# Kernel tuning notes

Measured on AMD Instinct MI355X. Metric: run time of the kernel, lower is better.

The kernel has to match this reference:

```python
import jax, jax.numpy as jnp
import numpy as np

B, T, D = 64, 2048, 256


def setup_inputs() -> dict:
    key = jax.random.key(0)
    k0, k1, k2, k3 = jax.random.split(key, 4)
    x0 = jax.random.normal(k0, (B, D), dtype=jnp.float32)
    I = jax.random.normal(k1, (B, T, D), dtype=jnp.float32)
    # Scale transition matrix so spectral norm < 1 (stable 2048-step recurrence),
    # mimicking eW = expm((W - I)*dt/tau) which is contractive for stable W.
    eW = jax.random.normal(k2, (D, D), dtype=jnp.float32) * (0.9 / np.sqrt(D))
    W_inv_eW = jax.random.normal(k3, (D, D), dtype=jnp.float32) * (1.0 / np.sqrt(D))
    return {"x0": x0, "I": I, "eW": eW, "W_inv_eW": W_inv_eW}


def reference(x0, I, eW, W_inv_eW):
    # x[:,0]=x0; x[:,t] = x[:,t-1] @ eW.T + I[:,t-1] @ W_inv_eW.T
    u = jnp.einsum('btd,sd->bts', I, W_inv_eW)  # [B, T, D], precompute input drive

    def step(x, u_t):
        x_new = x @ eW.T + u_t  # [B, D]
        return x_new, x_new

    # only u[:, :T-1] is consumed (x[:,t] uses I[:,t-1])
    _, xs = jax.lax.scan(step, x0, jnp.swapaxes(u[:, :-1], 0, 1))  # xs: [T-1, B, D]
    x = jnp.concatenate([x0[:, None, :], jnp.swapaxes(xs, 0, 1)], axis=1)  # [B, T, D]
    return x
```

## Files before the change

### kernel.cpp

```cpp
#include <hip/hip_runtime.h>
#include <stdint.h>
#include <stddef.h>


#define BATCH 64
#define TLEN 2048
#define DDIM 256
#define CHUNK 32
#define NCHUNK 64

typedef __attribute__((ext_vector_type(8))) short short8;
typedef __attribute__((ext_vector_type(4))) short short4_t;
typedef __attribute__((ext_vector_type(4))) float f32x4;

#define MFMA16(a, b, c) __builtin_amdgcn_mfma_f32_16x16x32_bf16((a), (b), (c), 0, 0, 0)
#define PIN8(x) asm volatile("" : "+v"(x))

__device__ __forceinline__ uint16_t f2bf(float f) {
  union { float f; uint32_t u; } v; v.f = f;
  return (uint16_t)((v.u + 0x7fffu + ((v.u >> 16) & 1u)) >> 16);
}
__device__ __forceinline__ float bf2f(uint16_t h) {
  union { uint32_t u; float f; } v; v.u = ((uint32_t)h) << 16;
  return v.f;
}

__device__ __forceinline__ void split8(const float* fv, short8& hi, short8& lo) {
#pragma unroll
  for (int j = 0; j < 8; ++j) {
    uint16_t hb = f2bf(fv[j]);
    hi[j] = (short)hb;
    lo[j] = (short)f2bf(fv[j] - bf2f(hb));
  }
}

__device__ __forceinline__ uint32_t swz(int row) {
  return ((uint32_t)((row & 7) << 4)) ^ ((uint32_t)(((row >> 3) & 1) << 7));
}

__device__ __forceinline__ void wg_barrier() {
  __builtin_amdgcn_sched_barrier(0);
  asm volatile("s_waitcnt lgkmcnt(0)" ::: "memory");
  __builtin_amdgcn_s_barrier();
  asm volatile("" ::: "memory");
  __builtin_amdgcn_sched_barrier(0);
}

#define WS_A_HI   (0)
#define WS_A_LO   (128 * 1024)
#define WS_WB_HI  (256 * 1024)
#define WS_WB_LO  (384 * 1024)
#define WS_M1F    (512 * 1024)
#define WS_M1_HI  (768 * 1024)
#define WS_M1_LO  (896 * 1024)
#define WS_M2F    (1024 * 1024)
#define WS_M2_HI  (1280 * 1024)
#define WS_M2_LO  (1408 * 1024)
#define WS_M3F    (1536 * 1024)
#define WS_M3_HI  (1792 * 1024)
#define WS_M3_LO  (1920 * 1024)
#define WS_ATF    (2048 * 1024)
#define WS_CNT    (2304 * 1024)
#define WS_S      (2560 * 1024)
#define WS_Y      (6656 * 1024)

__global__ void k_split(const float* __restrict__ eW, const float* __restrict__ Wi,
                        uint16_t* __restrict__ Ah, uint16_t* __restrict__ Al,
                        uint16_t* __restrict__ Wh, uint16_t* __restrict__ Wl,
                        float* __restrict__ AtF, unsigned int* __restrict__ cnt) {
  int idx = blockIdx.x * blockDim.x + threadIdx.x;
  if (idx == 0) *cnt = 0u;
  if (idx < 65536) {
    float v = eW[idx];
    uint16_t h = f2bf(v);
    Ah[idx] = h;
    Al[idx] = f2bf(v - bf2f(h));
    AtF[(idx & 255) * 256 + (idx >> 8)] = v;
  } else if (idx < 131072) {
    int i = idx - 65536;
    float v = Wi[i];
    uint16_t h = f2bf(v);
    Wh[i] = h;
    Wl[i] = f2bf(v - bf2f(h));
  }
}

__global__ __launch_bounds__(512) void k_power(
    const float* __restrict__ AtF, const uint16_t* __restrict__ Ah, const uint16_t* __restrict__ Al,
    float* __restrict__ M1f, uint16_t* __restrict__ M1h, uint16_t* __restrict__ M1l,
    float* __restrict__ M2f, uint16_t* __restrict__ M2h, uint16_t* __restrict__ M2l,
    float* __restrict__ M3f, uint16_t* __restrict__ M3h, uint16_t* __restrict__ M3l,
    unsigned int* __restrict__ cnt) {
  const int mf = blockIdx.x;
  const int tid = threadIdx.x;
  const int w = tid >> 6, l = tid & 63, l15 = l & 15, quad = l >> 4;
  const int ns = w * 32;

  auto mm = [&](const float* Af, const uint16_t* Bh, const uint16_t* Bl,
                float* Of, uint16_t* Oh, uint16_t* Ol) {
    f32x4 acc[2];
    acc[0] = {0.f, 0.f, 0.f, 0.f};
    acc[1] = {0.f, 0.f, 0.f, 0.f};
#pragma unroll
    for (int ks = 0; ks < 8; ++ks) {
      const float* ap = Af + (size_t)(mf * 16 + l15) * 256 + ks * 32 + quad * 8;
      f32x4 f0 = *reinterpret_cast<const f32x4*>(ap);
      f32x4 f1 = *reinterpret_cast<const f32x4*>(ap + 4);
      float fv[8] = {f0[0], f0[1], f0[2], f0[3], f1[0], f1[1], f1[2], f1[3]};
      short8 ah, al8;
      split8(fv, ah, al8);
#pragma unroll
      for (int nf = 0; nf < 2; ++nf) {
        const int off = (ns + nf * 16 + l15) * 256 + ks * 32 + quad * 8;
        short8 bhf = *reinterpret_cast<const short8*>(Bh + off);
        short8 blf = *reinterpret_cast<const short8*>(Bl + off);
        acc[nf] = MFMA16(ah, bhf, acc[nf]);
        acc[nf] = MFMA16(al8, bhf, acc[nf]);
        acc[nf] = MFMA16(ah, blf, acc[nf]);
      }
    }
#pragma unroll
    for (int nf = 0; nf < 2; ++nf)
#pragma unroll
      for (int r = 0; r < 4; ++r) {
        int row = mf * 16 + quad * 4 + r;
        int col = ns + nf * 16 + l15;
        float v = acc[nf][r];
        Of[(size_t)row * 256 + col] = v;
        uint16_t hb = f2bf(v);
        Oh[(size_t)col * 256 + row] = hb;
        Ol[(size_t)col * 256 + row] = f2bf(v - bf2f(hb));
      }
  };

  unsigned int target = 0;
  auto gbar = [&]() {
    __syncthreads();
    target += 16;
    if (tid == 0) {
      __hip_atomic_fetch_add(cnt, 1u, __ATOMIC_RELEASE, __HIP_MEMORY_SCOPE_AGENT);
      while (__hip_atomic_load(cnt, __ATOMIC_ACQUIRE, __HIP_MEMORY_SCOPE_AGENT) < target) {
      }
    }
    __syncthreads();
  };

  mm(AtF, Ah, Al, M2f, M2h, M2l);    gbar();
  mm(M2f, M2h, M2l, M3f, M3h, M3l);  gbar();
  mm(M3f, M3h, M3l, M2f, M2h, M2l);  gbar();
  mm(M2f, M2h, M2l, M3f, M3h, M3l);  gbar();
  mm(M3f, M3h, M3l, M1f, M1h, M1l);  gbar();
  mm(M1f, M1h, M1l, M2f, M2h, M2l);  gbar();
  mm(M2f, M1h, M1l, M3f, M3h, M3l);
}

__global__ __launch_bounds__(1024, 1) void k_u(const float* __restrict__ I,
                                               const uint16_t* __restrict__ Wh,
                                               const uint16_t* __restrict__ Wl,
                                               float* __restrict__ out) {
  const int tid = threadIdx.x;
  const int w = tid >> 6, l = tid & 63, l15 = l & 15, quad = l >> 4;
  const int ns = w * 16;
  __shared__ __align__(16) uint16_t sIh[2][4096];
  __shared__ __align__(16) uint16_t sIl[2][4096];

  short8 bh[8], bl[8];
#pragma unroll
  for (int ks = 0; ks < 8; ++ks) {
    const int off = (ns + l15) * 256 + ks * 32 + quad * 8;
    bh[ks] = *reinterpret_cast<const short8*>(Wh + off);
    bl[ks] = *reinterpret_cast<const short8*>(Wl + off);
    PIN8(bh[ks]);
    PIN8(bl[ks]);
  }

  const int srow = tid >> 6;
  const int sc0 = (tid & 63) * 4;
  const uint32_t wbyte = ((uint32_t)(srow * 512 + sc0 * 2)) ^ swz(srow);

  f32x4 ra, rb, rc, rd;
  auto loadI = [&](int tl, f32x4& dst) {
    const int b = tl >> 7, tt = tl & 127;
    dst = *reinterpret_cast<const f32x4*>(I + ((size_t)b * TLEN + tt * 16 + srow) * DDIM + sc0);
  };

  auto do_tile = [&](int tl, f32x4& cur, f32x4& pf, int q, bool pre) {
    if (pre) loadI(tl + 512, pf);
    short4_t hi4, lo4;
#pragma unroll
    for (int j = 0; j < 4; ++j) {
      uint16_t hb = f2bf(cur[j]);
      hi4[j] = (short)hb;
      lo4[j] = (short)f2bf(cur[j] - bf2f(hb));
    }
    *reinterpret_cast<short4_t*>(reinterpret_cast<char*>(sIh[q]) + wbyte) = hi4;
    *reinterpret_cast<short4_t*>(reinterpret_cast<char*>(sIl[q]) + wbyte) = lo4;
    wg_barrier();
    const int b = tl >> 7, tt = tl & 127;
    f32x4 acc = {0.f, 0.f, 0.f, 0.f};
    __builtin_amdgcn_s_setprio(1);
#pragma unroll
    for (int ks = 0; ks < 8; ++ks) {
      uint32_t rbyte = ((uint32_t)(l15 * 512 + ks * 64 + quad * 16)) ^ swz(l15);
      short8 ih = *reinterpret_cast<const short8*>((const char*)sIh[q] + rbyte);
      short8 il = *reinterpret_cast<const short8*>((const char*)sIl[q] + rbyte);
      acc = MFMA16(ih, bh[ks], acc);
      acc = MFMA16(il, bh[ks], acc);
      acc = MFMA16(ih, bl[ks], acc);
    }
    __builtin_amdgcn_s_setprio(0);
#pragma unroll
    for (int r = 0; r < 4; ++r) {
      int trow = tt * 16 + quad * 4 + r;
      if (trow <= TLEN - 2) {
        out[((size_t)b * TLEN + trow + 1) * DDIM + ns + l15] = acc[r];
      }
    }
  };

  const int tl0 = blockIdx.x;
  loadI(tl0, ra);
  loadI(tl0 + 256, rb);
#pragma unroll 1
  for (int it = 0; it < 32; it += 4) {
    do_tile(tl0 + (it + 0) * 256, ra, rc, 0, it + 2 < 32);
    do_tile(tl0 + (it + 1) * 256, rb, rd, 1, it + 3 < 32);
    do_tile(tl0 + (it + 2) * 256, rc, ra, 0, it + 4 < 32);
    do_tile(tl0 + (it + 3) * 256, rd, rb, 1, it + 5 < 32);
  }
}

__global__ __launch_bounds__(1024) void k_scan(const int pass,
                                               const uint16_t* __restrict__ Ah,
                                               const uint16_t* __restrict__ Al,
                                               float* __restrict__ xu,
                                               const float* __restrict__ Y,
                                               float* __restrict__ S) {
  const int tid = threadIdx.x;
  const int w = tid >> 6, l = tid & 63, l15 = l & 15, quad = l >> 4;
  const int ns = w * 16;
  const int c = blockIdx.x >> 2;
  const int rg = blockIdx.x & 3;
  __shared__ __align__(16) uint16_t sh[2][4096];
  __shared__ __align__(16) uint16_t sl[2][4096];

  const int t0 = c * CHUNK;
  const int nsteps = (t0 + CHUNK <= TLEN - 1) ? CHUNK : (TLEN - 1 - t0);

  float u0[4], u1[4], u2[4], u3[4], fin[4];
#pragma unroll
  for (int j = 0; j < 4; ++j) { u0[j] = 0.f; u1[j] = 0.f; u2[j] = 0.f; u3[j] = 0.f; fin[j] = 0.f; }

  auto issue_u = [&](int i, float (&dst)[4]) {
    if (i > nsteps) return;
#pragma unroll
    for (int r = 0; r < 4; ++r) {
      int b = rg * 16 + quad * 4 + r;
      dst[r] = xu[((size_t)b * TLEN + t0 + i) * DDIM + ns + l15];
    }
  };
  issue_u(1, u0);
  issue_u(2, u1);
  issue_u(3, u2);
  issue_u(4, u3);

  short8 fAh[8], fAl[8];
#pragma unroll
  for (int ks = 0; ks < 8; ++ks) {
    const int off = (ns + l15) * 256 + ks * 32 + quad * 8;
    fAh[ks] = *reinterpret_cast<const short8*>(Ah + off);
    fAl[ks] = *reinterpret_cast<const short8*>(Al + off);
    PIN8(fAh[ks]);
    PIN8(fAl[ks]);
  }

  for (int i = tid; i < 4096; i += 1024) {
    int row = i >> 8, k = i & 255;
    float v;
    if (pass == 1)
      v = 0.0f;
    else {
      v = Y[((size_t)c * 64 + rg * 16 + row) * DDIM + k];
      if (c == 0) xu[((size_t)(rg * 16 + row) * TLEN) * DDIM + k] = v;
    }
    uint16_t hb = f2bf(v);
    uint16_t lb = f2bf(v - bf2f(hb));
    uint32_t byte = ((uint32_t)(row * 512 + k * 2)) ^ swz(row);
    *(uint16_t*)((char*)sh[0] + byte) = hb;
    *(uint16_t*)((char*)sl[0] + byte) = lb;
  }
  wg_barrier();

  int p = 0;
  auto step = [&](int i, float (&ucur)[4]) {
    f32x4 acc = {0.f, 0.f, 0.f, 0.f};
    __builtin_amdgcn_s_setprio(1);
#pragma unroll
    for (int ks = 0; ks < 8; ++ks) {
      uint32_t byte = ((uint32_t)(l15 * 512 + ks * 64 + quad * 16)) ^ swz(l15);
      short8 xh = *reinterpret_cast<const short8*>((const char*)sh[p] + byte);
      short8 xl = *reinterpret_cast<const short8*>((const char*)sl[p] + byte);
      acc = MFMA16(xh, fAh[ks], acc);
      acc = MFMA16(xl, fAh[ks], acc);
      acc = MFMA16(xh, fAl[ks], acc);
    }
    __builtin_amdgcn_s_setprio(0);
#pragma unroll
    for (int r = 0; r < 4; ++r) fin[r] = acc[r] + ucur[r];
    issue_u(i + 4, ucur);
    if (pass == 2) {
#pragma unroll
      for (int r = 0; r < 4; ++r) {
        int b = rg * 16 + quad * 4 + r;
        xu[((size_t)b * TLEN + t0 + i) * DDIM + ns + l15] = fin[r];
      }
    }
    if (i < nsteps) {
#pragma unroll
      for (int r = 0; r < 4; ++r) {
        int row = quad * 4 + r, col = ns + l15;
        float v = fin[r];
        uint16_t hb = f2bf(v);
        uint16_t lb = f2bf(v - bf2f(hb));
        uint32_t byte = ((uint32_t)(row * 512 + col * 2)) ^ swz(row);
        *(uint16_t*)((char*)sh[p ^ 1] + byte) = hb;
        *(uint16_t*)((char*)sl[p ^ 1] + byte) = lb;
      }
      wg_barrier();
      p ^= 1;
    }
  };

  int i = 1;
  for (; i + 3 <= nsteps; i += 4) {
    step(i, u0);
    step(i + 1, u1);
    step(i + 2, u2);
    step(i + 3, u3);
  }
  if (i <= nsteps) { step(i, u0); ++i; }
  if (i <= nsteps) { step(i, u1); ++i; }
  if (i <= nsteps) { step(i, u2); ++i; }

  if (pass == 1) {
#pragma unroll
    for (int r = 0; r < 4; ++r) {
      int row = quad * 4 + r, col = ns + l15;
      S[((size_t)c * 64 + rg * 16 + row) * DDIM + col] = fin[r];
    }
  }
}

__global__ __launch_bounds__(512) void k_bnd(const float* __restrict__ x0,
                                             const float* __restrict__ S,
                                             const uint16_t* __restrict__ M1h, const uint16_t* __restrict__ M1l,
                                             const uint16_t* __restrict__ M2h, const uint16_t* __restrict__ M2l,
                                             const uint16_t* __restrict__ M3h, const uint16_t* __restrict__ M3l,
                                             float* __restrict__ Y) {
  const int c = blockIdx.x;
  const int tid = threadIdx.x;
  const int w = tid >> 6, l = tid & 63, l15 = l & 15, quad = l >> 4;
  const int ns = w * 32;
  f32x4 acc[4][2];
  const float* Tc = (c == 0) ? x0 : (S + (size_t)(c - 1) * 64 * 256);
#pragma unroll
  for (int mf = 0; mf < 4; ++mf)
#pragma unroll
    for (int nf = 0; nf < 2; ++nf)
#pragma unroll
      for (int r = 0; r < 4; ++r)
        acc[mf][nf][r] = Tc[(size_t)(mf * 16 + quad * 4 + r) * 256 + ns + nf * 16 + l15];

  for (int j = 1; j <= 3; ++j) {
    int k = c - j;
    if (k < 0) break;
    const float* Tp = (k == 0) ? x0 : (S + (size_t)(k - 1) * 64 * 256);
    const uint16_t* Bh = (j == 1) ? M1h : (j == 2) ? M2h : M3h;
    const uint16_t* Bl = (j == 1) ? M1l : (j == 2) ? M2l : M3l;
#pragma unroll
    for (int mf = 0; mf < 4; ++mf) {
#pragma unroll
      for (int ks = 0; ks < 8; ++ks) {
        const float* ap = Tp + (size_t)(mf * 16 + l15) * 256 + ks * 32 + quad * 8;
        f32x4 f0 = *reinterpret_cast<const f32x4*>(ap);
        f32x4 f1 = *reinterpret_cast<const f32x4*>(ap + 4);
        float fv[8] = {f0[0], f0[1], f0[2], f0[3], f1[0], f1[1], f1[2], f1[3]};
        short8 ah, al8;
        split8(fv, ah, al8);
#pragma unroll
        for (int nf = 0; nf < 2; ++nf) {
          const int off = (ns + nf * 16 + l15) * 256 + ks * 32 + quad * 8;
          short8 bhf = *reinterpret_cast<const short8*>(Bh + off);
          short8 blf = *reinterpret_cast<const short8*>(Bl + off);
          acc[mf][nf] = MFMA16(ah, bhf, acc[mf][nf]);
          acc[mf][nf] = MFMA16(al8, bhf, acc[mf][nf]);
          acc[mf][nf] = MFMA16(ah, blf, acc[mf][nf]);
        }
      }
    }
  }
#pragma unroll
  for (int mf = 0; mf < 4; ++mf)
#pragma unroll
    for (int nf = 0; nf < 2; ++nf)
#pragma unroll
      for (int r = 0; r < 4; ++r)
        Y[(size_t)c * 64 * 256 + (size_t)(mf * 16 + quad * 4 + r) * 256 + ns + nf * 16 + l15] =
            acc[mf][nf][r];
}

extern "C" void kernel_launch(void* const* d_in, const int* in_sizes, int n_in,
                              void* d_out, int out_size, void* d_ws, size_t ws_size,
                              hipStream_t stream) {
  (void)in_sizes; (void)n_in; (void)out_size; (void)ws_size;
  const float* x0 = (const float*)d_in[0];
  const float* I  = (const float*)d_in[1];
  const float* eW = (const float*)d_in[2];
  const float* Wi = (const float*)d_in[3];
  float* out = (float*)d_out;
  char* ws = (char*)d_ws;

  uint16_t* Ah  = (uint16_t*)(ws + WS_A_HI);
  uint16_t* Al  = (uint16_t*)(ws + WS_A_LO);
  uint16_t* Wh  = (uint16_t*)(ws + WS_WB_HI);
  uint16_t* Wl  = (uint16_t*)(ws + WS_WB_LO);
  float*    M1f = (float*)(ws + WS_M1F);
  uint16_t* M1h = (uint16_t*)(ws + WS_M1_HI);
  uint16_t* M1l = (uint16_t*)(ws + WS_M1_LO);
  float*    M2f = (float*)(ws + WS_M2F);
  uint16_t* M2h = (uint16_t*)(ws + WS_M2_HI);
  uint16_t* M2l = (uint16_t*)(ws + WS_M2_LO);
  float*    M3f = (float*)(ws + WS_M3F);
  uint16_t* M3h = (uint16_t*)(ws + WS_M3_HI);
  uint16_t* M3l = (uint16_t*)(ws + WS_M3_LO);
  float*    AtF = (float*)(ws + WS_ATF);
  unsigned int* cnt = (unsigned int*)(ws + WS_CNT);
  float*    S   = (float*)(ws + WS_S);
  float*    Y   = (float*)(ws + WS_Y);

  k_split<<<512, 256, 0, stream>>>(eW, Wi, Ah, Al, Wh, Wl, AtF, cnt);
  k_power<<<16, 512, 0, stream>>>(AtF, Ah, Al, M1f, M1h, M1l, M2f, M2h, M2l,
                                  M3f, M3h, M3l, cnt);
  k_u<<<256, 1024, 0, stream>>>(I, Wh, Wl, out);
  k_scan<<<256, 1024, 0, stream>>>(1, Ah, Al, out, Y, S);
  k_bnd<<<64, 512, 0, stream>>>(x0, S, M1h, M1l, M2h, M2l, M3h, M3l, Y);
  k_scan<<<256, 1024, 0, stream>>>(2, Ah, Al, out, Y, S);
}
```

Before: 342.3 us.

## Replace persistent power kernel with separate matmul launches and split MFMA accumulators

Removes the persistent k_power kernel, which used an atomic-counter grid barrier, and replaces it with seven k_mm256 launches, with kernel boundaries serving as the global sync. The power chain now launches after k_u rather than before. In k_u and k_scan, the three bf16 split-precision MFMA chains now use separate accumulators that are summed at the end. The separate accumulators break the serial MFMA dependency chain, which shortens latency per scan step. The cost is more kernel launches and slightly different rounding order.

```diff
diff --git a/kernel.cpp b/kernel.cpp
--- a/kernel.cpp
+++ b/kernel.cpp
@@ -60,16 +60,14 @@
 #define WS_M3_HI  (1792 * 1024)
 #define WS_M3_LO  (1920 * 1024)
 #define WS_ATF    (2048 * 1024)
-#define WS_CNT    (2304 * 1024)
 #define WS_S      (2560 * 1024)
 #define WS_Y      (6656 * 1024)
 
 __global__ void k_split(const float* __restrict__ eW, const float* __restrict__ Wi,
                         uint16_t* __restrict__ Ah, uint16_t* __restrict__ Al,
                         uint16_t* __restrict__ Wh, uint16_t* __restrict__ Wl,
-                        float* __restrict__ AtF, unsigned int* __restrict__ cnt) {
+                        float* __restrict__ AtF) {
   int idx = blockIdx.x * blockDim.x + threadIdx.x;
-  if (idx == 0) *cnt = 0u;
   if (idx < 65536) {
     float v = eW[idx];
     uint16_t h = f2bf(v);
@@ -85,75 +83,6 @@
   }
 }
 
-__global__ __launch_bounds__(512) void k_power(
-    const float* __restrict__ AtF, const uint16_t* __restrict__ Ah, const uint16_t* __restrict__ Al,
-    float* __restrict__ M1f, uint16_t* __restrict__ M1h, uint16_t* __restrict__ M1l,
-    float* __restrict__ M2f, uint16_t* __restrict__ M2h, uint16_t* __restrict__ M2l,
-    float* __restrict__ M3f, uint16_t* __restrict__ M3h, uint16_t* __restrict__ M3l,
-    unsigned int* __restrict__ cnt) {
-  const int mf = blockIdx.x;
-  const int tid = threadIdx.x;
-  const int w = tid >> 6, l = tid & 63, l15 = l & 15, quad = l >> 4;
-  const int ns = w * 32;
-
-  auto mm = [&](const float* Af, const uint16_t* Bh, const uint16_t* Bl,
-                float* Of, uint16_t* Oh, uint16_t* Ol) {
-    f32x4 acc[2];
-    acc[0] = {0.f, 0.f, 0.f, 0.f};
-    acc[1] = {0.f, 0.f, 0.f, 0.f};
-#pragma unroll
-    for (int ks = 0; ks < 8; ++ks) {
-      const float* ap = Af + (size_t)(mf * 16 + l15) * 256 + ks * 32 + quad * 8;
-      f32x4 f0 = *reinterpret_cast<const f32x4*>(ap);
-      f32x4 f1 = *reinterpret_cast<const f32x4*>(ap + 4);
-      float fv[8] = {f0[0], f0[1], f0[2], f0[3], f1[0], f1[1], f1[2], f1[3]};
-      short8 ah, al8;
-      split8(fv, ah, al8);
-#pragma unroll
-      for (int nf = 0; nf < 2; ++nf) {
-        const int off = (ns + nf * 16 + l15) * 256 + ks * 32 + quad * 8;
-        short8 bhf = *reinterpret_cast<const short8*>(Bh + off);
-        short8 blf = *reinterpret_cast<const short8*>(Bl + off);
-        acc[nf] = MFMA16(ah, bhf, acc[nf]);
-        acc[nf] = MFMA16(al8, bhf, acc[nf]);
-        acc[nf] = MFMA16(ah, blf, acc[nf]);
-      }
-    }
-#pragma unroll
-    for (int nf = 0; nf < 2; ++nf)
-#pragma unroll
-      for (int r = 0; r < 4; ++r) {
-        int row = mf * 16 + quad * 4 + r;
-        int col = ns + nf * 16 + l15;
-        float v = acc[nf][r];
-        Of[(size_t)row * 256 + col] = v;
-        uint16_t hb = f2bf(v);
-        Oh[(size_t)col * 256 + row] = hb;
-        Ol[(size_t)col * 256 + row] = f2bf(v - bf2f(hb));
-      }
-  };
-
-  unsigned int target = 0;
-  auto gbar = [&]() {
-    __syncthreads();
-    target += 16;
-    if (tid == 0) {
-      __hip_atomic_fetch_add(cnt, 1u, __ATOMIC_RELEASE, __HIP_MEMORY_SCOPE_AGENT);
-      while (__hip_atomic_load(cnt, __ATOMIC_ACQUIRE, __HIP_MEMORY_SCOPE_AGENT) < target) {
-      }
-    }
-    __syncthreads();
-  };
-
-  mm(AtF, Ah, Al, M2f, M2h, M2l);    gbar();
-  mm(M2f, M2h, M2l, M3f, M3h, M3l);  gbar();
-  mm(M3f, M3h, M3l, M2f, M2h, M2l);  gbar();
-  mm(M2f, M2h, M2l, M3f, M3h, M3l);  gbar();
-  mm(M3f, M3h, M3l, M1f, M1h, M1l);  gbar();
-  mm(M1f, M1h, M1l, M2f, M2h, M2l);  gbar();
-  mm(M2f, M1h, M1l, M3f, M3h, M3l);
-}
-
 __global__ __launch_bounds__(1024, 1) void k_u(const float* __restrict__ I,
                                                const uint16_t* __restrict__ Wh,
                                                const uint16_t* __restrict__ Wl,
@@ -197,23 +126,24 @@
     *reinterpret_cast<short4_t*>(reinterpret_cast<char*>(sIl[q]) + wbyte) = lo4;
     wg_barrier();
     const int b = tl >> 7, tt = tl & 127;
-    f32x4 acc = {0.f, 0.f, 0.f, 0.f};
+    f32x4 aH = {0.f, 0.f, 0.f, 0.f}, aL = {0.f, 0.f, 0.f, 0.f}, aM = {0.f, 0.f, 0.f, 0.f};
     __builtin_amdgcn_s_setprio(1);
 #pragma unroll
     for (int ks = 0; ks < 8; ++ks) {
       uint32_t rbyte = ((uint32_t)(l15 * 512 + ks * 64 + quad * 16)) ^ swz(l15);
       short8 ih = *reinterpret_cast<const short8*>((const char*)sIh[q] + rbyte);
       short8 il = *reinterpret_cast<const short8*>((const char*)sIl[q] + rbyte);
-      acc = MFMA16(ih, bh[ks], acc);
-      acc = MFMA16(il, bh[ks], acc);
-      acc = MFMA16(ih, bl[ks], acc);
+      aH = MFMA16(ih, bh[ks], aH);
+      aL = MFMA16(il, bh[ks], aL);
+      aM = MFMA16(ih, bl[ks], aM);
     }
     __builtin_amdgcn_s_setprio(0);
 #pragma unroll
     for (int r = 0; r < 4; ++r) {
       int trow = tt * 16 + quad * 4 + r;
       if (trow <= TLEN - 2) {
-        out[((size_t)b * TLEN + trow + 1) * DDIM + ns + l15] = acc[r];
+        out[((size_t)b * TLEN + trow + 1) * DDIM + ns + l15] =
+            aH[r] + (aL[r] + aM[r]);
       }
     }
   };
@@ -293,20 +223,20 @@
 
   int p = 0;
   auto step = [&](int i, float (&ucur)[4]) {
-    f32x4 acc = {0.f, 0.f, 0.f, 0.f};
+    f32x4 aH = {0.f, 0.f, 0.f, 0.f}, aL = {0.f, 0.f, 0.f, 0.f}, aM = {0.f, 0.f, 0.f, 0.f};
     __builtin_amdgcn_s_setprio(1);
 #pragma unroll
     for (int ks = 0; ks < 8; ++ks) {
       uint32_t byte = ((uint32_t)(l15 * 512 + ks * 64 + quad * 16)) ^ swz(l15);
       short8 xh = *reinterpret_cast<const short8*>((const char*)sh[p] + byte);
       short8 xl = *reinterpret_cast<const short8*>((const char*)sl[p] + byte);
-      acc = MFMA16(xh, fAh[ks], acc);
-      acc = MFMA16(xl, fAh[ks], acc);
-      acc = MFMA16(xh, fAl[ks], acc);
+      aH = MFMA16(xh, fAh[ks], aH);
+      aL = MFMA16(xl, fAh[ks], aL);
+      aM = MFMA16(xh, fAl[ks], aM);
     }
     __builtin_amdgcn_s_setprio(0);
 #pragma unroll
-    for (int r = 0; r < 4; ++r) fin[r] = acc[r] + ucur[r];
+    for (int r = 0; r < 4; ++r) fin[r] = (aH[r] + (aL[r] + aM[r])) + ucur[r];
     issue_u(i + 4, ucur);
     if (pass == 2) {
 #pragma unroll
@@ -349,6 +279,52 @@
       S[((size_t)c * 64 + rg * 16 + row) * DDIM + col] = fin[r];
     }
   }
+}
+
+__global__ __launch_bounds__(512) void k_mm256(const float* __restrict__ Af,
+                                               const uint16_t* __restrict__ Bh,
+                                               const uint16_t* __restrict__ Bl,
+                                               float* __restrict__ Of,
+                                               uint16_t* __restrict__ Oh,
+                                               uint16_t* __restrict__ Ol) {
+  const int mf = blockIdx.x;
+  const int tid = threadIdx.x;
+  const int w = tid >> 6, l = tid & 63, l15 = l & 15, quad = l >> 4;
+  const int ns = w * 32;
+  f32x4 acc[2];
+  acc[0] = {0.f, 0.f, 0.f, 0.f};
+  acc[1] = {0.f, 0.f, 0.f, 0.f};
+
+#pragma unroll
+  for (int ks = 0; ks < 8; ++ks) {
+    const float* ap = Af + (size_t)(mf * 16 + l15) * 256 + ks * 32 + quad * 8;
+    f32x4 f0 = *reinterpret_cast<const f32x4*>(ap);
+    f32x4 f1 = *reinterpret_cast<const f32x4*>(ap + 4);
+    float fv[8] = {f0[0], f0[1], f0[2], f0[3], f1[0], f1[1], f1[2], f1[3]};
+    short8 ah, al8;
+    split8(fv, ah, al8);
+#pragma unroll
+    for (int nf = 0; nf < 2; ++nf) {
+      const int off = (ns + nf * 16 + l15) * 256 + ks * 32 + quad * 8;
+      short8 bhf = *reinterpret_cast<const short8*>(Bh + off);
+      short8 blf = *reinterpret_cast<const short8*>(Bl + off);
+      acc[nf] = MFMA16(ah, bhf, acc[nf]);
+      acc[nf] = MFMA16(al8, bhf, acc[nf]);
+      acc[nf] = MFMA16(ah, blf, acc[nf]);
+    }
+  }
+#pragma unroll
+  for (int nf = 0; nf < 2; ++nf)
+#pragma unroll
+    for (int r = 0; r < 4; ++r) {
+      int row = mf * 16 + quad * 4 + r;
+      int col = ns + nf * 16 + l15;
+      float v = acc[nf][r];
+      Of[(size_t)row * 256 + col] = v;
+      uint16_t hb = f2bf(v);
+      Oh[(size_t)col * 256 + row] = hb;
+      Ol[(size_t)col * 256 + row] = f2bf(v - bf2f(hb));
+    }
 }
 
 __global__ __launch_bounds__(512) void k_bnd(const float* __restrict__ x0,
@@ -434,14 +410,18 @@
   uint16_t* M3h = (uint16_t*)(ws + WS_M3_HI);
   uint16_t* M3l = (uint16_t*)(ws + WS_M3_LO);
   float*    AtF = (float*)(ws + WS_ATF);
-  unsigned int* cnt = (unsigned int*)(ws + WS_CNT);
   float*    S   = (float*)(ws + WS_S);
   float*    Y   = (float*)(ws + WS_Y);
 
-  k_split<<<512, 256, 0, stream>>>(eW, Wi, Ah, Al, Wh, Wl, AtF, cnt);
-  k_power<<<16, 512, 0, stream>>>(AtF, Ah, Al, M1f, M1h, M1l, M2f, M2h, M2l,
-                                  M3f, M3h, M3l, cnt);
+  k_split<<<512, 256, 0, stream>>>(eW, Wi, Ah, Al, Wh, Wl, AtF);
   k_u<<<256, 1024, 0, stream>>>(I, Wh, Wl, out);
+  k_mm256<<<16, 512, 0, stream>>>(AtF, Ah, Al, M2f, M2h, M2l);
+  k_mm256<<<16, 512, 0, stream>>>(M2f, M2h, M2l, M3f, M3h, M3l);
+  k_mm256<<<16, 512, 0, stream>>>(M3f, M3h, M3l, M2f, M2h, M2l);
+  k_mm256<<<16, 512, 0, stream>>>(M2f, M2h, M2l, M3f, M3h, M3l);
+  k_mm256<<<16, 512, 0, stream>>>(M3f, M3h, M3l, M1f, M1h, M1l);
+  k_mm256<<<16, 512, 0, stream>>>(M1f, M1h, M1l, M2f, M2h, M2l);
+  k_mm256<<<16, 512, 0, stream>>>(M2f, M1h, M1l, M3f, M3h, M3l);
   k_scan<<<256, 1024, 0, stream>>>(1, Ah, Al, out, Y, S);
   k_bnd<<<64, 512, 0, stream>>>(x0, S, M1h, M1l, M2h, M2l, M3h, M3l, Y);
   k_scan<<<256, 1024, 0, stream>>>(2, Ah, Al, out, Y, S);
```

Measured after the change: 381.2 us. +11.4%, slower.
